# Kernel optimization log

Measured on AMD Instinct MI355X. Metric: run time of the kernel, lower is better.

## Reference

```python
import jax, jax.numpy as jnp
import numpy as np

N_EL = 16
N_NUC = 4
N_FEATS = 32
CUTOFF = 10.0
ION_POT = 0.5
ALPHA = 1.0
BATCH = 32768
HIDDEN = 64
I_IDX, J_IDX = np.triu_indices(N_EL, 1)  # electron pairs i<j
N_PAIRS = N_EL * N_NUC + N_EL * (N_EL - 1) // 2
D_IN = N_PAIRS * N_FEATS


def ssp(x):
    # shifted softplus: softplus(x) - log(2), so ssp(0) = 0
    return jax.nn.softplus(x) - jnp.log(2.0).astype(x.dtype)


def setup_inputs() -> dict:
    key = jax.random.key(0)
    ks = jax.random.split(key, 9)
    rs = jax.random.normal(ks[0], (BATCH, N_EL, 3), jnp.float32) * 2.0
    coords = jax.random.normal(ks[1], (N_NUC, 3), jnp.float32)
    charges = jnp.arange(1, N_NUC + 1, dtype=jnp.float32)
    W1 = jax.random.normal(ks[2], (D_IN, HIDDEN), jnp.float32) / jnp.sqrt(D_IN)
    b1 = jnp.zeros((HIDDEN,), jnp.float32)
    W2 = jax.random.normal(ks[3], (HIDDEN, HIDDEN), jnp.float32) / jnp.sqrt(HIDDEN)
    b2 = jnp.zeros((HIDDEN,), jnp.float32)
    W3 = jax.random.normal(ks[4], (HIDDEN, 1), jnp.float32) / jnp.sqrt(HIDDEN)
    b3 = jnp.zeros((1,), jnp.float32)
    return {"rs": rs, "coords": coords, "charges": charges,
            "W1": W1, "b1": b1, "W2": W2, "b2": b2, "W3": W3, "b3": b3}


def reference(rs, coords, charges, W1, b1, W2, b2, W3, b3):
    B = rs.shape[0]
    # electron-nucleus distances: [B, n_el, n_nuc]
    diff_nuc = rs[:, :, None, :] - coords[None, None, :, :]
    dists_nuc = jnp.sqrt(jnp.sum(diff_nuc * diff_nuc, axis=-1))
    # electron-electron distances for pairs i<j: [B, n_el*(n_el-1)//2]
    diff_el = rs[:, I_IDX, :] - rs[:, J_IDX, :]
    dists_el = jnp.sqrt(jnp.sum(diff_el * diff_el, axis=-1))
    dists = jnp.concatenate([dists_nuc.reshape(B, -1), dists_el], axis=1)  # [B, N_PAIRS]
    # Gaussian distance basis expansion
    qs = jnp.linspace(0.0, 1.0, N_FEATS, dtype=rs.dtype)
    mus = CUTOFF * qs ** 2
    sigmas = (1.0 + CUTOFF * qs) / 7.0
    xs = jnp.exp(-((dists[..., None] - mus) ** 2) / sigmas ** 2)  # [B, N_PAIRS, N_FEATS]
    xs = xs.reshape(B, -1)
    # small MLP with shifted-softplus activations
    h = ssp(xs @ W1 + b1)
    h = ssp(h @ W2 + b2)
    ys = (h @ W3 + b3)[:, 0]
    # nuclear asymptotic factor
    decay = jnp.sqrt(2.0 * ION_POT)
    terms = (charges[None, None, :] * dists_nuc + decay * ALPHA * dists_nuc ** 2) / (1.0 + ALPHA * dists_nuc)
    asymp = jnp.exp(-jnp.sum(terms, axis=(1, 2)))
    return jnp.exp(ys) * asymp
```

## Files before the change

kernel.cpp:

```cpp
#include <hip/hip_runtime.h>
#include <math.h>

#define N_EL    16
#define N_NUC   4
#define N_FEATS 32
#define N_PAIRS 184
#define HIDDEN  64
#define TB      32
#define BLOCK   256
#define DLD     185
#define H1LD    68
#define TPW     23
#define WS_PART_OFF (1 << 19)

typedef int   intx8    __attribute__((ext_vector_type(8)));
typedef float floatx16 __attribute__((ext_vector_type(16)));

__device__ __forceinline__ float exp2_raw(float x) {
    float r;
    asm("v_exp_f32 %0, %1" : "=v"(r) : "v"(x));
    return r;
}

__constant__ unsigned char c_I[120] = {
    0,0,0,0,0,0,0,0,0,0,0,0,0,0,0,
    1,1,1,1,1,1,1,1,1,1,1,1,1,1,
    2,2,2,2,2,2,2,2,2,2,2,2,2,
    3,3,3,3,3,3,3,3,3,3,3,3,
    4,4,4,4,4,4,4,4,4,4,4,
    5,5,5,5,5,5,5,5,5,5,
    6,6,6,6,6,6,6,6,6,
    7,7,7,7,7,7,7,7,
    8,8,8,8,8,8,8,
    9,9,9,9,9,9,
    10,10,10,10,10,
    11,11,11,11,
    12,12,12,
    13,13,
    14
};
__constant__ unsigned char c_J[120] = {
    1,2,3,4,5,6,7,8,9,10,11,12,13,14,15,
    2,3,4,5,6,7,8,9,10,11,12,13,14,15,
    3,4,5,6,7,8,9,10,11,12,13,14,15,
    4,5,6,7,8,9,10,11,12,13,14,15,
    5,6,7,8,9,10,11,12,13,14,15,
    6,7,8,9,10,11,12,13,14,15,
    7,8,9,10,11,12,13,14,15,
    8,9,10,11,12,13,14,15,
    9,10,11,12,13,14,15,
    10,11,12,13,14,15,
    11,12,13,14,15,
    12,13,14,15,
    13,14,15,
    14,15,
    15
};

__device__ __forceinline__ float ssp(float x) {
    float a = fabsf(x);
    return fmaxf(x, 0.0f) + log1pf(__expf(-a)) - 0.69314718056f;
}
__device__ __forceinline__ float redg(float v) {
    v += __shfl_xor(v, 1);
    v += __shfl_xor(v, 2);
    v += __shfl_xor(v, 4);
    return v;
}

__global__ __launch_bounds__(256)
void prep_w1_kernel(const float* __restrict__ W1, intx8* __restrict__ ws)
{
    __shared__ float w[2 * N_FEATS * HIDDEN];
    const int t = blockIdx.x;
    const float* src = W1 + (size_t)(2 * t) * (N_FEATS * HIDDEN);
    for (int k = threadIdx.x; k < 2 * N_FEATS * HIDDEN; k += 256) w[k] = src[k];
    __syncthreads();

    const int tid = threadIdx.x;
    if (tid >= 128) return;
    const int lane = tid & 63;
    const int nh   = tid >> 6;
    const int lh   = lane >> 5;
    const int col  = nh * 32 + (lane & 31);
    const int fb   = lh * 16;
    intx8 frag;
#pragma unroll
    for (int r = 0; r < 8; ++r) {
        const int pair = r >> 2;
        const int fo   = fb + ((r & 3) << 2);
        const float v0 = 64.0f * w[(pair * N_FEATS + fo + 0) * 64 + col];
        const float v1 = 64.0f * w[(pair * N_FEATS + fo + 1) * 64 + col];
        const float v2 = 64.0f * w[(pair * N_FEATS + fo + 2) * 64 + col];
        const float v3 = 64.0f * w[(pair * N_FEATS + fo + 3) * 64 + col];
        int d = __builtin_amdgcn_cvt_pk_fp8_f32(v0, v1, 0, false);
        d     = __builtin_amdgcn_cvt_pk_fp8_f32(v2, v3, d, true);
        frag[r] = d;
    }
    ws[(size_t)(t * 2 + nh) * 64 + lane] = frag;
}

__global__ __launch_bounds__(BLOCK)
void wfnet_gemm(const float* __restrict__ rs,
                const float* __restrict__ coords,
                const intx8* __restrict__ ws,
                float* __restrict__ partials)
{
    __shared__ float lds_rs[TB * N_EL * 3];
    __shared__ float lds_dist[TB * DLD];

    const int tid  = threadIdx.x;
    const int wave = tid >> 6;
    const int lane = tid & 63;
    const int m    = lane & 31;
    const int lh   = lane >> 5;

    {
        const float* rs_blk = rs + (size_t)blockIdx.x * (TB * N_EL * 3);
        for (int k = tid; k < TB * N_EL * 3; k += BLOCK) lds_rs[k] = rs_blk[k];
    }
    __syncthreads();

    {
        const int bl = tid >> 3, g = tid & 7;
        const float* myrs = lds_rs + bl * (N_EL * 3);
        float* dst = lds_dist + bl * DLD;
        for (int i = 0; i < 8; ++i) {
            const int p = g + 8 * i;
            const int e = p >> 2, n = p & 3;
            const float dx = myrs[e * 3 + 0] - coords[n * 3 + 0];
            const float dy = myrs[e * 3 + 1] - coords[n * 3 + 1];
            const float dz = myrs[e * 3 + 2] - coords[n * 3 + 2];
            dst[p] = sqrtf(dx * dx + dy * dy + dz * dz);
        }
        for (int i = 0; i < 15; ++i) {
            const int q  = g + 8 * i;
            const int ei = 3 * (int)c_I[q], ej = 3 * (int)c_J[q];
            const float dx = myrs[ei + 0] - myrs[ej + 0];
            const float dy = myrs[ei + 1] - myrs[ej + 1];
            const float dz = myrs[ei + 2] - myrs[ej + 2];
            dst[64 + q] = sqrtf(dx * dx + dy * dy + dz * dz);
        }
    }
    __syncthreads();

    const int f0 = lh * 16;
#define MKC(P, FF) float P##1, P##0; { \
    const float fq = (float)(FF) * (1.0f / 31.0f); \
    const float mu = 10.0f * fq * fq; \
    const float is = 7.0f / (1.0f + 10.0f * fq); \
    P##1 = is * 1.2011224087864498f; \
    P##0 = -mu * P##1; }
    MKC(F0_,  f0 + 0)  MKC(F1_,  f0 + 1)  MKC(F2_,  f0 + 2)  MKC(F3_,  f0 + 3)
    MKC(F4_,  f0 + 4)  MKC(F5_,  f0 + 5)  MKC(F6_,  f0 + 6)  MKC(F7_,  f0 + 7)
    MKC(F8_,  f0 + 8)  MKC(F9_,  f0 + 9)  MKC(F10_, f0 + 10) MKC(F11_, f0 + 11)
    MKC(F12_, f0 + 12) MKC(F13_, f0 + 13) MKC(F14_, f0 + 14) MKC(F15_, f0 + 15)
#undef MKC

    floatx16 accA = {};
    floatx16 accB = {};
    const intx8* wq = ws + ((size_t)(wave * TPW) * 128 + lane);
    const float* drow = lds_dist + m * DLD + wave * (2 * TPW);

#define XO(dd, P) ({ const float t_ = fmaf(dd, P##1, P##0); exp2_raw(t_ * -t_); })
#define MKA8(AV, dx0, dx1) \
    intx8 AV; { int dw_; \
    dw_   = __builtin_amdgcn_cvt_pk_fp8_f32(XO(dx0,F0_),  XO(dx0,F1_),  0,  false); \
    AV[0] = __builtin_amdgcn_cvt_pk_fp8_f32(XO(dx0,F2_),  XO(dx0,F3_),  dw_, true); \
    dw_   = __builtin_amdgcn_cvt_pk_fp8_f32(XO(dx0,F4_),  XO(dx0,F5_),  0,  false); \
    AV[1] = __builtin_amdgcn_cvt_pk_fp8_f32(XO(dx0,F6_),  XO(dx0,F7_),  dw_, true); \
    dw_   = __builtin_amdgcn_cvt_pk_fp8_f32(XO(dx0,F8_),  XO(dx0,F9_),  0,  false); \
    AV[2] = __builtin_amdgcn_cvt_pk_fp8_f32(XO(dx0,F10_), XO(dx0,F11_), dw_, true); \
    dw_   = __builtin_amdgcn_cvt_pk_fp8_f32(XO(dx0,F12_), XO(dx0,F13_), 0,  false); \
    AV[3] = __builtin_amdgcn_cvt_pk_fp8_f32(XO(dx0,F14_), XO(dx0,F15_), dw_, true); \
    dw_   = __builtin_amdgcn_cvt_pk_fp8_f32(XO(dx1,F0_),  XO(dx1,F1_),  0,  false); \
    AV[4] = __builtin_amdgcn_cvt_pk_fp8_f32(XO(dx1,F2_),  XO(dx1,F3_),  dw_, true); \
    dw_   = __builtin_amdgcn_cvt_pk_fp8_f32(XO(dx1,F4_),  XO(dx1,F5_),  0,  false); \
    AV[5] = __builtin_amdgcn_cvt_pk_fp8_f32(XO(dx1,F6_),  XO(dx1,F7_),  dw_, true); \
    dw_   = __builtin_amdgcn_cvt_pk_fp8_f32(XO(dx1,F8_),  XO(dx1,F9_),  0,  false); \
    AV[6] = __builtin_amdgcn_cvt_pk_fp8_f32(XO(dx1,F10_), XO(dx1,F11_), dw_, true); \
    dw_   = __builtin_amdgcn_cvt_pk_fp8_f32(XO(dx1,F12_), XO(dx1,F13_), 0,  false); \
    AV[7] = __builtin_amdgcn_cvt_pk_fp8_f32(XO(dx1,F14_), XO(dx1,F15_), dw_, true); }
#define KROUND(AV, Q0, Q1) { \
    accA = __builtin_amdgcn_mfma_scale_f32_32x32x64_f8f6f4( \
               AV, Q0, accA, 0, 0, 0, 0x7F7F7F7F, 0, 0x79797979); \
    accB = __builtin_amdgcn_mfma_scale_f32_32x32x64_f8f6f4( \
               AV, Q1, accB, 0, 0, 0, 0x7F7F7F7F, 0, 0x79797979); }

    intx8 pA0 = wq[0],   pA1 = wq[64];
    intx8 pB0 = wq[128], pB1 = wq[192];
    float dA0 = drow[0], dA1 = drow[1];
    float dB0 = drow[2], dB1 = drow[3];

    for (int it = 0; it < 10; ++it) {
        const intx8* wn = wq + 256;
        const float eA0 = drow[4 * it + 4], eA1 = drow[4 * it + 5];
        const float eB0 = drow[4 * it + 6], eB1 = drow[4 * it + 7];

        { MKA8(av, dA0, dA1) KROUND(av, pA0, pA1) }
        pA0 = wn[0]; pA1 = wn[64];

        { MKA8(bv, dB0, dB1) KROUND(bv, pB0, pB1) }
        pB0 = wn[128]; pB1 = wn[192];

        wq = wn;
        dA0 = eA0; dA1 = eA1; dB0 = eB0; dB1 = eB1;
    }
    {
        const intx8* wn = wq + 256;
        const float eA0 = drow[44], eA1 = drow[45];
        { MKA8(av, dA0, dA1) KROUND(av, pA0, pA1) }
        pA0 = wn[0]; pA1 = wn[64];
        { MKA8(bv, dB0, dB1) KROUND(bv, pB0, pB1) }
        { MKA8(cv, eA0, eA1) KROUND(cv, pA0, pA1) }
    }
#undef KROUND
#undef MKA8
#undef XO

    float* pdst = partials + ((size_t)blockIdx.x * 4 + wave) * 2048;
#pragma unroll
    for (int rg = 0; rg < 16; ++rg) {
        const int el = (rg & 3) + 8 * (rg >> 2) + 4 * lh;
        pdst[el * 64 + m]      = accA[rg];
        pdst[el * 64 + 32 + m] = accB[rg];
    }
}

__global__ __launch_bounds__(BLOCK)
void wfnet_tail(const float* __restrict__ rs,
                const float* __restrict__ coords,
                const float* __restrict__ charges,
                const float* __restrict__ partials,
                const float* __restrict__ b1,
                const float* __restrict__ W2,
                const float* __restrict__ b2,
                const float* __restrict__ W3,
                const float* __restrict__ b3,
                float* __restrict__ out)
{
    __shared__ float lds_rs[TB * N_EL * 3];
    __shared__ float lds_h1[TB * H1LD];

    const int tid = threadIdx.x;
    const int el  = tid >> 3;
    const int g   = tid & 7;
    const int b   = blockIdx.x * TB + el;

    {
        const float* rs_blk = rs + (size_t)blockIdx.x * (TB * N_EL * 3);
        for (int k = tid; k < TB * N_EL * 3; k += BLOCK) lds_rs[k] = rs_blk[k];
    }

    {
        const float* pb = partials + (size_t)blockIdx.x * 8192 + el * 64 + g * 8;
        const float4 p00 = ((const float4*)(pb + 0 * 2048))[0];
        const float4 p01 = ((const float4*)(pb + 0 * 2048))[1];
        const float4 p10 = ((const float4*)(pb + 1 * 2048))[0];
        const float4 p11 = ((const float4*)(pb + 1 * 2048))[1];
        const float4 p20 = ((const float4*)(pb + 2 * 2048))[0];
        const float4 p21 = ((const float4*)(pb + 2 * 2048))[1];
        const float4 p30 = ((const float4*)(pb + 3 * 2048))[0];
        const float4 p31 = ((const float4*)(pb + 3 * 2048))[1];
        const float4 ba = ((const float4*)(b1 + g * 8))[0];
        const float4 bb = ((const float4*)(b1 + g * 8))[1];
        float* h1w = lds_h1 + el * H1LD + g * 8;
        h1w[0] = ssp(p00.x + p10.x + p20.x + p30.x + ba.x);
        h1w[1] = ssp(p00.y + p10.y + p20.y + p30.y + ba.y);
        h1w[2] = ssp(p00.z + p10.z + p20.z + p30.z + ba.z);
        h1w[3] = ssp(p00.w + p10.w + p20.w + p30.w + ba.w);
        h1w[4] = ssp(p01.x + p11.x + p21.x + p31.x + bb.x);
        h1w[5] = ssp(p01.y + p11.y + p21.y + p31.y + bb.y);
        h1w[6] = ssp(p01.z + p11.z + p21.z + p31.z + bb.z);
        h1w[7] = ssp(p01.w + p11.w + p21.w + p31.w + bb.w);
    }

    float asy = 0.0f;
    __syncthreads();
    {
        const float* myrs = lds_rs + el * (N_EL * 3);
        const float4 ch = *(const float4*)charges;
#pragma unroll
        for (int i = 0; i < 8; ++i) {
            const int p = g + 8 * i;
            const int e = p >> 2, n = p & 3;
            const float dx = myrs[e * 3 + 0] - coords[n * 3 + 0];
            const float dy = myrs[e * 3 + 1] - coords[n * 3 + 1];
            const float dz = myrs[e * 3 + 2] - coords[n * 3 + 2];
            const float d = sqrtf(dx * dx + dy * dy + dz * dz);
            const float Z = (n < 2) ? ((n == 0) ? ch.x : ch.y)
                                    : ((n == 2) ? ch.z : ch.w);
            asy += (Z * d + d * d) / (1.0f + d);
        }
    }
    asy = redg(asy);

    const float4* __restrict__ W2v = (const float4*)W2;
    const float4* __restrict__ b2v = (const float4*)b2;
    const int wbi = g * 2;
    const float4 b2a = b2v[wbi], b2b = b2v[wbi + 1];
    float s0 = b2a.x, s1 = b2a.y, s2 = b2a.z, s3 = b2a.w;
    float s4 = b2b.x, s5 = b2b.y, s6 = b2b.z, s7 = b2b.w;

    const float* __restrict__ h1row = lds_h1 + el * H1LD;
    for (int k = 0; k < HIDDEN; ++k) {
        const float hk  = h1row[k];
        const float4 wa = W2v[k * 16 + wbi];
        const float4 wb = W2v[k * 16 + wbi + 1];
        s0 = fmaf(hk, wa.x, s0); s1 = fmaf(hk, wa.y, s1);
        s2 = fmaf(hk, wa.z, s2); s3 = fmaf(hk, wa.w, s3);
        s4 = fmaf(hk, wb.x, s4); s5 = fmaf(hk, wb.y, s5);
        s6 = fmaf(hk, wb.z, s6); s7 = fmaf(hk, wb.w, s7);
    }

    const float4* __restrict__ W3v = (const float4*)W3;
    const float4 w3a = W3v[wbi], w3b = W3v[wbi + 1];
    float part = ssp(s0) * w3a.x + ssp(s1) * w3a.y
               + ssp(s2) * w3a.z + ssp(s3) * w3a.w
               + ssp(s4) * w3b.x + ssp(s5) * w3b.y
               + ssp(s6) * w3b.z + ssp(s7) * w3b.w;
    part = redg(part);

    if (g == 0) {
        const float ys = part + b3[0];
        out[b] = __expf(ys) * __expf(-asy);
    }
}

extern "C" void kernel_launch(void* const* d_in, const int* in_sizes, int n_in,
                              void* d_out, int out_size, void* d_ws, size_t ws_size,
                              hipStream_t stream) {
    const float* rs      = (const float*)d_in[0];
    const float* coords  = (const float*)d_in[1];
    const float* charges = (const float*)d_in[2];
    const float* W1      = (const float*)d_in[3];
    const float* b1      = (const float*)d_in[4];
    const float* W2      = (const float*)d_in[5];
    const float* b2      = (const float*)d_in[6];
    const float* W3      = (const float*)d_in[7];
    const float* b3      = (const float*)d_in[8];
    float* out = (float*)d_out;

    const int batch = in_sizes[0] / (N_EL * 3);
    intx8* w1f8     = (intx8*)d_ws;
    float* partials = (float*)((char*)d_ws + WS_PART_OFF);

    prep_w1_kernel<<<N_PAIRS / 2, 256, 0, stream>>>(W1, w1f8);
    wfnet_gemm<<<batch / TB, BLOCK, 0, stream>>>(rs, coords, w1f8, partials);
    wfnet_tail<<<batch / TB, BLOCK, 0, stream>>>(rs, coords, charges, partials,
                                                 b1, W2, b2, W3, b3, out);
}
```

Before: 147.0 us.

## Split distance computation into separate kernel and use raw exp/log in ssp

Distance computation moves out of the GEMM kernel into its own kernel, which writes a pair-major distance buffer to global workspace. The GEMM kernel then reads distances straight from global memory with coalesced loads, drops its LDS buffers and barriers, and declares a minimum of 6 blocks per SM via launch bounds to raise occupancy. The shifted softplus now uses raw v_exp/v_log instructions instead of log1pf/__expf. In exchange this adds a kernel launch and a global round trip of the distance array (~24MB), and the raw log loses some accuracy for small z.

```diff
diff --git a/kernel.cpp b/kernel.cpp
--- a/kernel.cpp
+++ b/kernel.cpp
@@ -8,10 +8,10 @@
 #define HIDDEN  64
 #define TB      32
 #define BLOCK   256
-#define DLD     185
 #define H1LD    68
 #define TPW     23
-#define WS_PART_OFF (1 << 19)
+#define WS_DIST_OFF 393216
+#define WS_PART_OFF (393216 + 24117248)
 
 typedef int   intx8    __attribute__((ext_vector_type(8)));
 typedef float floatx16 __attribute__((ext_vector_type(16)));
@@ -19,6 +19,11 @@
 __device__ __forceinline__ float exp2_raw(float x) {
     float r;
     asm("v_exp_f32 %0, %1" : "=v"(r) : "v"(x));
+    return r;
+}
+__device__ __forceinline__ float log2_raw(float x) {
+    float r;
+    asm("v_log_f32 %0, %1" : "=v"(r) : "v"(x));
     return r;
 }
 
@@ -58,8 +63,9 @@
 };
 
 __device__ __forceinline__ float ssp(float x) {
-    float a = fabsf(x);
-    return fmaxf(x, 0.0f) + log1pf(__expf(-a)) - 0.69314718056f;
+    const float z = exp2_raw(-fabsf(x) * 1.4426950408889634f);
+    const float w = log2_raw(1.0f + z);
+    return fmaxf(x, 0.0f) + fmaf(0.6931471805599453f, w, -0.69314718056f);
 }
 __device__ __forceinline__ float redg(float v) {
     v += __shfl_xor(v, 1);
@@ -100,49 +106,52 @@
     ws[(size_t)(t * 2 + nh) * 64 + lane] = frag;
 }
 
-__global__ __launch_bounds__(BLOCK)
-void wfnet_gemm(const float* __restrict__ rs,
-                const float* __restrict__ coords,
+__global__ __launch_bounds__(256)
+void dist_kernel(const float* __restrict__ rs,
+                 const float* __restrict__ coords,
+                 float* __restrict__ dw)
+{
+    __shared__ float lds_rs[TB * N_EL * 3];
+    const int tid = threadIdx.x;
+    {
+        const float* rs_blk = rs + (size_t)blockIdx.x * (TB * N_EL * 3);
+        for (int k = tid; k < TB * N_EL * 3; k += 256) lds_rs[k] = rs_blk[k];
+    }
+    __syncthreads();
+
+    const int el = tid & 31, g = tid >> 5;
+    const float* myrs = lds_rs + el * (N_EL * 3);
+    float* base = dw + (size_t)blockIdx.x * (N_PAIRS * 32) + el;
+#pragma unroll
+    for (int i = 0; i < 23; ++i) {
+        const int p = g + 8 * i;
+        float dx, dy, dz;
+        if (p < 64) {
+            const int e = p >> 2, n = p & 3;
+            dx = myrs[e * 3 + 0] - coords[n * 3 + 0];
+            dy = myrs[e * 3 + 1] - coords[n * 3 + 1];
+            dz = myrs[e * 3 + 2] - coords[n * 3 + 2];
+        } else {
+            const int q  = p - 64;
+            const int ei = 3 * (int)c_I[q], ej = 3 * (int)c_J[q];
+            dx = myrs[ei + 0] - myrs[ej + 0];
+            dy = myrs[ei + 1] - myrs[ej + 1];
+            dz = myrs[ei + 2] - myrs[ej + 2];
+        }
+        base[p * 32] = sqrtf(dx * dx + dy * dy + dz * dz);
+    }
+}
+
+__global__ __launch_bounds__(BLOCK, 6)
+void wfnet_gemm(const float* __restrict__ dw,
                 const intx8* __restrict__ ws,
                 float* __restrict__ partials)
 {
-    __shared__ float lds_rs[TB * N_EL * 3];
-    __shared__ float lds_dist[TB * DLD];
-
     const int tid  = threadIdx.x;
     const int wave = tid >> 6;
     const int lane = tid & 63;
     const int m    = lane & 31;
     const int lh   = lane >> 5;
-
-    {
-        const float* rs_blk = rs + (size_t)blockIdx.x * (TB * N_EL * 3);
-        for (int k = tid; k < TB * N_EL * 3; k += BLOCK) lds_rs[k] = rs_blk[k];
-    }
-    __syncthreads();
-
-    {
-        const int bl = tid >> 3, g = tid & 7;
-        const float* myrs = lds_rs + bl * (N_EL * 3);
-        float* dst = lds_dist + bl * DLD;
-        for (int i = 0; i < 8; ++i) {
-            const int p = g + 8 * i;
-            const int e = p >> 2, n = p & 3;
-            const float dx = myrs[e * 3 + 0] - coords[n * 3 + 0];
-            const float dy = myrs[e * 3 + 1] - coords[n * 3 + 1];
-            const float dz = myrs[e * 3 + 2] - coords[n * 3 + 2];
-            dst[p] = sqrtf(dx * dx + dy * dy + dz * dz);
-        }
-        for (int i = 0; i < 15; ++i) {
-            const int q  = g + 8 * i;
-            const int ei = 3 * (int)c_I[q], ej = 3 * (int)c_J[q];
-            const float dx = myrs[ei + 0] - myrs[ej + 0];
-            const float dy = myrs[ei + 1] - myrs[ej + 1];
-            const float dz = myrs[ei + 2] - myrs[ej + 2];
-            dst[64 + q] = sqrtf(dx * dx + dy * dy + dz * dz);
-        }
-    }
-    __syncthreads();
 
     const int f0 = lh * 16;
 #define MKC(P, FF) float P##1, P##0; { \
@@ -160,7 +169,8 @@
     floatx16 accA = {};
     floatx16 accB = {};
     const intx8* wq = ws + ((size_t)(wave * TPW) * 128 + lane);
-    const float* drow = lds_dist + m * DLD + wave * (2 * TPW);
+    const float* dp = dw + (size_t)blockIdx.x * (N_PAIRS * 32)
+                         + (wave * 2 * TPW) * 32 + m;
 
 #define XO(dd, P) ({ const float t_ = fmaf(dd, P##1, P##0); exp2_raw(t_ * -t_); })
 #define MKA8(AV, dx0, dx1) \
@@ -189,13 +199,14 @@
 
     intx8 pA0 = wq[0],   pA1 = wq[64];
     intx8 pB0 = wq[128], pB1 = wq[192];
-    float dA0 = drow[0], dA1 = drow[1];
-    float dB0 = drow[2], dB1 = drow[3];
+    float dA0 = dp[0],  dA1 = dp[32];
+    float dB0 = dp[64], dB1 = dp[96];
 
     for (int it = 0; it < 10; ++it) {
         const intx8* wn = wq + 256;
-        const float eA0 = drow[4 * it + 4], eA1 = drow[4 * it + 5];
-        const float eB0 = drow[4 * it + 6], eB1 = drow[4 * it + 7];
+        const float* dn = dp + 128;
+        const float eA0 = dn[0],  eA1 = dn[32];
+        const float eB0 = dn[64], eB1 = dn[96];
 
         { MKA8(av, dA0, dA1) KROUND(av, pA0, pA1) }
         pA0 = wn[0]; pA1 = wn[64];
@@ -203,12 +214,12 @@
         { MKA8(bv, dB0, dB1) KROUND(bv, pB0, pB1) }
         pB0 = wn[128]; pB1 = wn[192];
 
-        wq = wn;
+        wq = wn; dp = dn;
         dA0 = eA0; dA1 = eA1; dB0 = eB0; dB1 = eB1;
     }
     {
         const intx8* wn = wq + 256;
-        const float eA0 = drow[44], eA1 = drow[45];
+        const float eA0 = dp[128], eA1 = dp[160];
         { MKA8(av, dA0, dA1) KROUND(av, pA0, pA1) }
         pA0 = wn[0]; pA1 = wn[64];
         { MKA8(bv, dB0, dB1) KROUND(bv, pB0, pB1) }
@@ -343,10 +354,12 @@
 
     const int batch = in_sizes[0] / (N_EL * 3);
     intx8* w1f8     = (intx8*)d_ws;
+    float* dists    = (float*)((char*)d_ws + WS_DIST_OFF);
     float* partials = (float*)((char*)d_ws + WS_PART_OFF);
 
     prep_w1_kernel<<<N_PAIRS / 2, 256, 0, stream>>>(W1, w1f8);
-    wfnet_gemm<<<batch / TB, BLOCK, 0, stream>>>(rs, coords, w1f8, partials);
+    dist_kernel<<<batch / TB, 256, 0, stream>>>(rs, coords, dists);
+    wfnet_gemm<<<batch / TB, BLOCK, 0, stream>>>(dists, w1f8, partials);
     wfnet_tail<<<batch / TB, BLOCK, 0, stream>>>(rs, coords, charges, partials,
                                                  b1, W2, b2, W3, b3, out);
 }
```

Result: slower. 328.7 us (+123.6%).
